# Performance work log

Hardware: AMD Instinct MI355X
Metric: run time of the kernel (lower is better)

Reference implementation:

```python
import jax, jax.numpy as jnp
import numpy as np

MARGIN = 0.5
N_CLASSES = 100

def setup_inputs() -> dict:
    key = jax.random.key(0)
    k1, k2 = jax.random.split(key)
    n, d = 8192, 128
    inputs = jax.random.normal(k1, (n, d), dtype=jnp.float32)
    targets = jax.random.randint(k2, (n,), 0, N_CLASSES, dtype=jnp.int64)
    return {"inputs": inputs, "targets": targets}

def reference(inputs, targets):
    # pairwise squared euclidean distances: [n, n]
    sq = jnp.sum(inputs * inputs, axis=1)  # [n]
    dist = sq[:, None] + sq[None, :] - 2.0 * (inputs @ inputs.T)
    dist = jnp.maximum(dist, 0.0)
    # positive mask: same label (diagonal included, matching original)
    mask = targets[:, None] == targets[None, :]  # [n, n] bool
    big = jnp.float32(1e30)
    dist_ap = jnp.max(jnp.where(mask, dist, -big), axis=1)  # hardest positive per row
    dist_an = jnp.min(jnp.where(mask, big, dist), axis=1)   # hardest negative per row
    loss = jnp.sum(jax.nn.relu(dist_ap - dist_an + MARGIN))
    return loss
```

## Files before the change

### kernel.cpp

```cpp
#include <hip/hip_runtime.h>
#include <hip/hip_bf16.h>

#define D 128
#define MARGIN 0.5f
#define NSPLIT 16
#define JSPAN 512

typedef __attribute__((ext_vector_type(8))) short bf16x8;
typedef __attribute__((ext_vector_type(4))) float f32x4;

__global__ void prep_kernel(const float* __restrict__ x,
                            float* __restrict__ sq,
                            unsigned* __restrict__ ap,
                            unsigned* __restrict__ an,
                            __hip_bfloat16* __restrict__ xb,
                            float* __restrict__ out, int n) {
    int tid = threadIdx.x;
    int row = blockIdx.x * 4 + (tid >> 6);
    int lane = tid & 63;
    const float2* xr = (const float2*)(x + (size_t)row * D);
    float2 v = xr[lane];
    __hip_bfloat162 b2;
    b2.x = __float2bfloat16(v.x);
    b2.y = __float2bfloat16(v.y);
    ((__hip_bfloat162*)(xb + (size_t)row * D))[lane] = b2;
    float s = v.x * v.x + v.y * v.y;
    #pragma unroll
    for (int o = 32; o > 0; o >>= 1) s += __shfl_xor(s, o, 64);
    if (lane == 0) {
        sq[row] = s;
        ap[row] = 0u;
        an[row] = 0x7F800000u;
    }
    if (blockIdx.x == 0 && tid == 0) *out = 0.0f;
}

__launch_bounds__(256, 4)
__global__ void gram_kernel(const __hip_bfloat16* __restrict__ xb,
                            const float* __restrict__ sq,
                            const int* __restrict__ tgt,
                            unsigned* __restrict__ ap,
                            unsigned* __restrict__ an, int n) {
    __shared__ __align__(16) __hip_bfloat16 Bs[2][64 * D];
    __shared__ float sqs[JSPAN];
    __shared__ int   tgs[JSPAN];

    const int tid  = threadIdx.x;
    const int wid  = tid >> 6;
    const int lane = tid & 63;
    const int quad = lane >> 4;
    const int l    = lane & 15;
    const int i0   = blockIdx.x * 128;
    const int jspan = n / NSPLIT;
    const int njit  = jspan / 64;
    const int j0    = blockIdx.y * jspan;
    const int rowbase = i0 + wid * 32;

    bf16x8 afrag[2][4];
    {
        const __hip_bfloat16* abase = xb + (size_t)(rowbase + l) * D + quad * 8;
        #pragma unroll
        for (int mt = 0; mt < 2; ++mt)
            #pragma unroll
            for (int ks = 0; ks < 4; ++ks)
                afrag[mt][ks] = *(const bf16x8*)(abase + (size_t)mt * 16 * D + ks * 32);
    }

    int li[2][4];
    #pragma unroll
    for (int mt = 0; mt < 2; ++mt)
        #pragma unroll
        for (int reg = 0; reg < 4; ++reg)
            li[mt][reg] = tgt[rowbase + mt * 16 + quad * 4 + reg];

    float lap[8], lan[8];
    #pragma unroll
    for (int k = 0; k < 8; ++k) { lap[k] = -1e30f; lan[k] = 1e30f; }

    const int q0 = wid * 256;
    const char* xbb = (const char*)xb;

    #define PREFETCH(jt0, buf)                                                \
        do {                                                                  \
            _Pragma("unroll")                                                 \
            for (int i_ = 0; i_ < 4; ++i_) {                                  \
                int q_ = q0 + i_ * 64 + lane;                                 \
                int r_ = q_ >> 4;                                             \
                int c_ = (q_ & 15) ^ (r_ & 15);                               \
                const char* g_ = xbb + (size_t)((jt0) + r_) * 256             \
                                     + (size_t)c_ * 16;                       \
                char* l_ = (char*)&Bs[buf][0] + (size_t)(q0 + i_ * 64) * 16;  \
                __builtin_amdgcn_global_load_lds(                             \
                    (const __attribute__((address_space(1))) void*)g_,        \
                    (__attribute__((address_space(3))) void*)l_, 16, 0, 0);   \
            }                                                                 \
        } while (0)

    PREFETCH(j0, 0);
    sqs[tid]       = sq[j0 + tid];
    sqs[tid + 256] = sq[j0 + tid + 256];
    tgs[tid]       = tgt[j0 + tid];
    tgs[tid + 256] = tgt[j0 + tid + 256];
    __syncthreads();

    for (int jj = 0; jj < njit; ++jj) {
        const int cur = jj & 1;
        if (jj < njit - 1) PREFETCH(j0 + (jj + 1) * 64, cur ^ 1);

        const char* Bb = (const char*)&Bs[cur][0];
        const int jb = jj * 64;
        #pragma unroll
        for (int jt = 0; jt < 4; ++jt) {
            f32x4 acc0 = (f32x4){0.f, 0.f, 0.f, 0.f};
            f32x4 acc1 = (f32x4){0.f, 0.f, 0.f, 0.f};
            #pragma unroll
            for (int ks = 0; ks < 4; ++ks) {
                int q = (jt * 16 + l) * 16 + ((ks * 4 + quad) ^ l);
                bf16x8 bfr = *(const bf16x8*)(Bb + (size_t)q * 16);
                acc0 = __builtin_amdgcn_mfma_f32_16x16x32_bf16(afrag[0][ks], bfr, acc0, 0, 0, 0);
                acc1 = __builtin_amdgcn_mfma_f32_16x16x32_bf16(afrag[1][ks], bfr, acc1, 0, 0, 0);
            }
            float sjc = sqs[jb + jt * 16 + l];
            int   tjc = tgs[jb + jt * 16 + l];
            #pragma unroll
            for (int reg = 0; reg < 4; ++reg) {
                float t0 = fmaf(-2.0f, acc0[reg], sjc);
                float t1 = fmaf(-2.0f, acc1[reg], sjc);
                bool s0 = (li[0][reg] == tjc);
                bool s1 = (li[1][reg] == tjc);
                lap[reg]     = fmaxf(lap[reg],     s0 ? t0 : -1e30f);
                lan[reg]     = fminf(lan[reg],     s0 ? 1e30f : t0);
                lap[4 + reg] = fmaxf(lap[4 + reg], s1 ? t1 : -1e30f);
                lan[4 + reg] = fminf(lan[4 + reg], s1 ? 1e30f : t1);
            }
        }

        __syncthreads();
    }
    #undef PREFETCH

    #pragma unroll
    for (int mt = 0; mt < 2; ++mt)
        #pragma unroll
        for (int reg = 0; reg < 4; ++reg) {
            float p = lap[mt * 4 + reg], q = lan[mt * 4 + reg];
            #pragma unroll
            for (int o = 1; o < 16; o <<= 1) {
                p = fmaxf(p, __shfl_xor(p, o, 64));
                q = fminf(q, __shfl_xor(q, o, 64));
            }
            if (l == mt * 4 + reg) {
                int gi = rowbase + mt * 16 + quad * 4 + reg;
                float s = sq[gi];
                atomicMax(&ap[gi], __float_as_uint(fmaxf(s + p, 0.0f)));
                atomicMin(&an[gi], __float_as_uint(fmaxf(s + q, 0.0f)));
            }
        }
}

__global__ void final_kernel(const unsigned* __restrict__ ap,
                             const unsigned* __restrict__ an,
                             float* __restrict__ out, int n) {
    int i = blockIdx.x * blockDim.x + threadIdx.x;
    float v = 0.f;
    if (i < n) {
        float p = __uint_as_float(ap[i]);
        float q = __uint_as_float(an[i]);
        v = fmaxf(p - q + MARGIN, 0.0f);
    }
    #pragma unroll
    for (int o = 32; o > 0; o >>= 1) v += __shfl_xor(v, o, 64);
    __shared__ float ws[4];
    int lane = threadIdx.x & 63, w = threadIdx.x >> 6;
    if (lane == 0) ws[w] = v;
    __syncthreads();
    if (threadIdx.x == 0) atomicAdd(out, ws[0] + ws[1] + ws[2] + ws[3]);
}

extern "C" void kernel_launch(void* const* d_in, const int* in_sizes, int n_in,
                              void* d_out, int out_size, void* d_ws, size_t ws_size,
                              hipStream_t stream) {
    const float* x   = (const float*)d_in[0];
    const int*   tgt = (const int*)d_in[1];
    float* out = (float*)d_out;
    const int n = in_sizes[1];

    float*          sq = (float*)d_ws;
    unsigned*       ap = (unsigned*)((char*)d_ws + (size_t)n * 4);
    unsigned*       an = ap + n;
    __hip_bfloat16* xb = (__hip_bfloat16*)((char*)d_ws + (size_t)n * 12);

    prep_kernel<<<n / 4, 256, 0, stream>>>(x, sq, ap, an, xb, out, n);
    dim3 grid(n / 128, NSPLIT);
    gram_kernel<<<grid, 256, 0, stream>>>(xb, sq, tgt, ap, an, n);
    final_kernel<<<n / 256, 256, 0, stream>>>(ap, an, out, n);
}
```

Measured before the change: 88.50 us.

## Use 4-stage 32-row LDS ring with fine-grained vmcnt waits and MFMA priority

Replaces the 2-buffer, 64-row double buffering with a 4-slot ring of 32-row tiles, prefetched three tiles ahead via global_load_lds. Explicit s_waitcnt vmcnt counts and raw s_barrier replace the per-iteration __syncthreads, so more loads stay in flight and barriers no longer drain all memory traffic. It also raises wave priority around the MFMA block with s_setprio. The loop count is hardcoded to 16 tiles of 32 rows, tying the kernel to n/NSPLIT == JSPAN == 512. The hand-written waitcnt counts must also match the compiler's actual instruction stream.

```diff
diff --git a/kernel.cpp b/kernel.cpp
--- a/kernel.cpp
+++ b/kernel.cpp
@@ -41,7 +41,7 @@
                             const int* __restrict__ tgt,
                             unsigned* __restrict__ ap,
                             unsigned* __restrict__ an, int n) {
-    __shared__ __align__(16) __hip_bfloat16 Bs[2][64 * D];
+    __shared__ __align__(16) __hip_bfloat16 Bs[4][32 * D];
     __shared__ float sqs[JSPAN];
     __shared__ int   tgs[JSPAN];
 
@@ -51,9 +51,7 @@
     const int quad = lane >> 4;
     const int l    = lane & 15;
     const int i0   = blockIdx.x * 128;
-    const int jspan = n / NSPLIT;
-    const int njit  = jspan / 64;
-    const int j0    = blockIdx.y * jspan;
+    const int j0   = blockIdx.y * JSPAN;
     const int rowbase = i0 + wid * 32;
 
     bf16x8 afrag[2][4];
@@ -77,67 +75,88 @@
     #pragma unroll
     for (int k = 0; k < 8; ++k) { lap[k] = -1e30f; lan[k] = 1e30f; }
 
-    const int q0 = wid * 256;
     const char* xbb = (const char*)xb;
 
-    #define PREFETCH(jt0, buf)                                                \
+    #define PREF_HALF(h)                                                      \
         do {                                                                  \
+            const int s_ = (h) & 3;                                           \
             _Pragma("unroll")                                                 \
-            for (int i_ = 0; i_ < 4; ++i_) {                                  \
-                int q_ = q0 + i_ * 64 + lane;                                 \
+            for (int i_ = 0; i_ < 2; ++i_) {                                  \
+                int q_ = wid * 128 + i_ * 64 + lane;                          \
                 int r_ = q_ >> 4;                                             \
                 int c_ = (q_ & 15) ^ (r_ & 15);                               \
-                const char* g_ = xbb + (size_t)((jt0) + r_) * 256             \
+                const char* g_ = xbb + (size_t)(j0 + (h) * 32 + r_) * 256     \
                                      + (size_t)c_ * 16;                       \
-                char* l_ = (char*)&Bs[buf][0] + (size_t)(q0 + i_ * 64) * 16;  \
+                char* l_ = (char*)Bs + (size_t)s_ * 8192                      \
+                         + (size_t)(wid * 128 + i_ * 64) * 16;                \
                 __builtin_amdgcn_global_load_lds(                             \
                     (const __attribute__((address_space(1))) void*)g_,        \
                     (__attribute__((address_space(3))) void*)l_, 16, 0, 0);   \
             }                                                                 \
         } while (0)
 
-    PREFETCH(j0, 0);
+    #define COMP_HALF(h)                                                      \
+        do {                                                                  \
+            const char* Bb_ = (const char*)Bs + (size_t)((h) & 3) * 8192;     \
+            _Pragma("unroll")                                                 \
+            for (int jt = 0; jt < 2; ++jt) {                                  \
+                f32x4 acc0 = (f32x4){0.f, 0.f, 0.f, 0.f};                     \
+                f32x4 acc1 = (f32x4){0.f, 0.f, 0.f, 0.f};                     \
+                __builtin_amdgcn_s_setprio(1);                                \
+                _Pragma("unroll")                                             \
+                for (int ks = 0; ks < 4; ++ks) {                              \
+                    int q = (jt * 16 + l) * 16 + ((ks * 4 + quad) ^ l);       \
+                    bf16x8 bfr = *(const bf16x8*)(Bb_ + (size_t)q * 16);      \
+                    acc0 = __builtin_amdgcn_mfma_f32_16x16x32_bf16(           \
+                        afrag[0][ks], bfr, acc0, 0, 0, 0);                    \
+                    acc1 = __builtin_amdgcn_mfma_f32_16x16x32_bf16(           \
+                        afrag[1][ks], bfr, acc1, 0, 0, 0);                    \
+                }                                                             \
+                __builtin_amdgcn_s_setprio(0);                                \
+                int jb_ = (h) * 32 + jt * 16;                                 \
+                float sjc = sqs[jb_ + l];                                     \
+                int   tjc = tgs[jb_ + l];                                     \
+                _Pragma("unroll")                                             \
+                for (int reg = 0; reg < 4; ++reg) {                           \
+                    float t0 = fmaf(-2.0f, acc0[reg], sjc);                   \
+                    float t1 = fmaf(-2.0f, acc1[reg], sjc);                   \
+                    bool s0 = (li[0][reg] == tjc);                            \
+                    bool s1 = (li[1][reg] == tjc);                            \
+                    lap[reg]     = fmaxf(lap[reg],     s0 ? t0 : -1e30f);     \
+                    lan[reg]     = fminf(lan[reg],     s0 ? 1e30f : t0);      \
+                    lap[4 + reg] = fmaxf(lap[4 + reg], s1 ? t1 : -1e30f);     \
+                    lan[4 + reg] = fminf(lan[4 + reg], s1 ? 1e30f : t1);      \
+                }                                                             \
+            }                                                                 \
+        } while (0)
+
+    PREF_HALF(0);
+    PREF_HALF(1);
+    PREF_HALF(2);
     sqs[tid]       = sq[j0 + tid];
     sqs[tid + 256] = sq[j0 + tid + 256];
     tgs[tid]       = tgt[j0 + tid];
     tgs[tid + 256] = tgt[j0 + tid + 256];
-    __syncthreads();
-
-    for (int jj = 0; jj < njit; ++jj) {
-        const int cur = jj & 1;
-        if (jj < njit - 1) PREFETCH(j0 + (jj + 1) * 64, cur ^ 1);
-
-        const char* Bb = (const char*)&Bs[cur][0];
-        const int jb = jj * 64;
-        #pragma unroll
-        for (int jt = 0; jt < 4; ++jt) {
-            f32x4 acc0 = (f32x4){0.f, 0.f, 0.f, 0.f};
-            f32x4 acc1 = (f32x4){0.f, 0.f, 0.f, 0.f};
-            #pragma unroll
-            for (int ks = 0; ks < 4; ++ks) {
-                int q = (jt * 16 + l) * 16 + ((ks * 4 + quad) ^ l);
-                bf16x8 bfr = *(const bf16x8*)(Bb + (size_t)q * 16);
-                acc0 = __builtin_amdgcn_mfma_f32_16x16x32_bf16(afrag[0][ks], bfr, acc0, 0, 0, 0);
-                acc1 = __builtin_amdgcn_mfma_f32_16x16x32_bf16(afrag[1][ks], bfr, acc1, 0, 0, 0);
-            }
-            float sjc = sqs[jb + jt * 16 + l];
-            int   tjc = tgs[jb + jt * 16 + l];
-            #pragma unroll
-            for (int reg = 0; reg < 4; ++reg) {
-                float t0 = fmaf(-2.0f, acc0[reg], sjc);
-                float t1 = fmaf(-2.0f, acc1[reg], sjc);
-                bool s0 = (li[0][reg] == tjc);
-                bool s1 = (li[1][reg] == tjc);
-                lap[reg]     = fmaxf(lap[reg],     s0 ? t0 : -1e30f);
-                lan[reg]     = fminf(lan[reg],     s0 ? 1e30f : t0);
-                lap[4 + reg] = fmaxf(lap[4 + reg], s1 ? t1 : -1e30f);
-                lan[4 + reg] = fminf(lan[4 + reg], s1 ? 1e30f : t1);
-            }
-        }
-
-        __syncthreads();
-    }
-    #undef PREFETCH
+    asm volatile("s_waitcnt lgkmcnt(0)" ::: "memory");
+
+    for (int h = 0; h < 14; ++h) {
+        asm volatile("s_waitcnt vmcnt(4)" ::: "memory");
+        __builtin_amdgcn_s_barrier();
+        asm volatile("" ::: "memory");
+        if (h < 13) PREF_HALF(h + 3);
+        COMP_HALF(h);
+    }
+    asm volatile("s_waitcnt vmcnt(2)" ::: "memory");
+    __builtin_amdgcn_s_barrier();
+    asm volatile("" ::: "memory");
+    COMP_HALF(14);
+    asm volatile("s_waitcnt vmcnt(0)" ::: "memory");
+    __builtin_amdgcn_s_barrier();
+    asm volatile("" ::: "memory");
+    COMP_HALF(15);
+
+    #undef PREF_HALF
+    #undef COMP_HALF
 
     #pragma unroll
     for (int mt = 0; mt < 2; ++mt)
```

New measurement: 86.67 us. 2.1% less time.

## Load B fragments directly from global memory and replace atomics with per-split partials

Applied to the files above, without the earlier changes.

Drops the LDS double-buffered B tile and its per-iteration barrier. Each wave now reads its B fragments straight from global memory (expected to hit L2, since the bf16 matrix is small), processing 32 columns per iteration with interleaved MFMAs under raised wave priority. The global atomicMax/atomicMin on ap/an are replaced by plain stores into per-split partial arrays, which the final kernel reduces across the 16 splits. The cost is redundant global/L2 traffic, because the four waves in a block each reload the same B rows, plus a larger workspace.

```diff
diff --git a/kernel.cpp b/kernel.cpp
--- a/kernel.cpp
+++ b/kernel.cpp
@@ -11,8 +11,6 @@
 
 __global__ void prep_kernel(const float* __restrict__ x,
                             float* __restrict__ sq,
-                            unsigned* __restrict__ ap,
-                            unsigned* __restrict__ an,
                             __hip_bfloat16* __restrict__ xb,
                             float* __restrict__ out, int n) {
     int tid = threadIdx.x;
@@ -27,11 +25,7 @@
     float s = v.x * v.x + v.y * v.y;
     #pragma unroll
     for (int o = 32; o > 0; o >>= 1) s += __shfl_xor(s, o, 64);
-    if (lane == 0) {
-        sq[row] = s;
-        ap[row] = 0u;
-        an[row] = 0x7F800000u;
-    }
+    if (lane == 0) sq[row] = s;
     if (blockIdx.x == 0 && tid == 0) *out = 0.0f;
 }
 
@@ -39,9 +33,8 @@
 __global__ void gram_kernel(const __hip_bfloat16* __restrict__ xb,
                             const float* __restrict__ sq,
                             const int* __restrict__ tgt,
-                            unsigned* __restrict__ ap,
-                            unsigned* __restrict__ an, int n) {
-    __shared__ __align__(16) __hip_bfloat16 Bs[2][64 * D];
+                            float* __restrict__ pap,
+                            float* __restrict__ pan, int n) {
     __shared__ float sqs[JSPAN];
     __shared__ int   tgs[JSPAN];
 
@@ -51,10 +44,13 @@
     const int quad = lane >> 4;
     const int l    = lane & 15;
     const int i0   = blockIdx.x * 128;
-    const int jspan = n / NSPLIT;
-    const int njit  = jspan / 64;
-    const int j0    = blockIdx.y * jspan;
+    const int j0   = blockIdx.y * JSPAN;
     const int rowbase = i0 + wid * 32;
+
+    sqs[tid]       = sq[j0 + tid];
+    sqs[tid + 256] = sq[j0 + tid + 256];
+    tgs[tid]       = tgt[j0 + tid];
+    tgs[tid + 256] = tgt[j0 + tid + 256];
 
     bf16x8 afrag[2][4];
     {
@@ -77,67 +73,53 @@
     #pragma unroll
     for (int k = 0; k < 8; ++k) { lap[k] = -1e30f; lan[k] = 1e30f; }
 
-    const int q0 = wid * 256;
-    const char* xbb = (const char*)xb;
-
-    #define PREFETCH(jt0, buf)                                                \
-        do {                                                                  \
-            _Pragma("unroll")                                                 \
-            for (int i_ = 0; i_ < 4; ++i_) {                                  \
-                int q_ = q0 + i_ * 64 + lane;                                 \
-                int r_ = q_ >> 4;                                             \
-                int c_ = (q_ & 15) ^ (r_ & 15);                               \
-                const char* g_ = xbb + (size_t)((jt0) + r_) * 256             \
-                                     + (size_t)c_ * 16;                       \
-                char* l_ = (char*)&Bs[buf][0] + (size_t)(q0 + i_ * 64) * 16;  \
-                __builtin_amdgcn_global_load_lds(                             \
-                    (const __attribute__((address_space(1))) void*)g_,        \
-                    (__attribute__((address_space(3))) void*)l_, 16, 0, 0);   \
-            }                                                                 \
-        } while (0)
-
-    PREFETCH(j0, 0);
-    sqs[tid]       = sq[j0 + tid];
-    sqs[tid + 256] = sq[j0 + tid + 256];
-    tgs[tid]       = tgt[j0 + tid];
-    tgs[tid + 256] = tgt[j0 + tid + 256];
     __syncthreads();
 
-    for (int jj = 0; jj < njit; ++jj) {
-        const int cur = jj & 1;
-        if (jj < njit - 1) PREFETCH(j0 + (jj + 1) * 64, cur ^ 1);
+    const char* xbb = (const char*)xb + (size_t)j0 * 256;
 
-        const char* Bb = (const char*)&Bs[cur][0];
-        const int jb = jj * 64;
+    for (int it = 0; it < 16; ++it) {
+        const int jb = it * 32;
+        bf16x8 bfr[2][4];
         #pragma unroll
-        for (int jt = 0; jt < 4; ++jt) {
-            f32x4 acc0 = (f32x4){0.f, 0.f, 0.f, 0.f};
-            f32x4 acc1 = (f32x4){0.f, 0.f, 0.f, 0.f};
+        for (int sub = 0; sub < 2; ++sub)
             #pragma unroll
-            for (int ks = 0; ks < 4; ++ks) {
-                int q = (jt * 16 + l) * 16 + ((ks * 4 + quad) ^ l);
-                bf16x8 bfr = *(const bf16x8*)(Bb + (size_t)q * 16);
-                acc0 = __builtin_amdgcn_mfma_f32_16x16x32_bf16(afrag[0][ks], bfr, acc0, 0, 0, 0);
-                acc1 = __builtin_amdgcn_mfma_f32_16x16x32_bf16(afrag[1][ks], bfr, acc1, 0, 0, 0);
-            }
-            float sjc = sqs[jb + jt * 16 + l];
-            int   tjc = tgs[jb + jt * 16 + l];
+            for (int ks = 0; ks < 4; ++ks)
+                bfr[sub][ks] = *(const bf16x8*)(
+                    xbb + (size_t)(jb + sub * 16 + l) * 256 + (ks * 4 + quad) * 16);
+
+        f32x4 acc[2][2];
+        #pragma unroll
+        for (int sub = 0; sub < 2; ++sub)
             #pragma unroll
-            for (int reg = 0; reg < 4; ++reg) {
-                float t0 = fmaf(-2.0f, acc0[reg], sjc);
-                float t1 = fmaf(-2.0f, acc1[reg], sjc);
-                bool s0 = (li[0][reg] == tjc);
-                bool s1 = (li[1][reg] == tjc);
-                lap[reg]     = fmaxf(lap[reg],     s0 ? t0 : -1e30f);
-                lan[reg]     = fminf(lan[reg],     s0 ? 1e30f : t0);
-                lap[4 + reg] = fmaxf(lap[4 + reg], s1 ? t1 : -1e30f);
-                lan[4 + reg] = fminf(lan[4 + reg], s1 ? 1e30f : t1);
-            }
+            for (int mt = 0; mt < 2; ++mt)
+                acc[sub][mt] = (f32x4){0.f, 0.f, 0.f, 0.f};
+
+        __builtin_amdgcn_s_setprio(1);
+        #pragma unroll
+        for (int ks = 0; ks < 4; ++ks)
+            #pragma unroll
+            for (int sub = 0; sub < 2; ++sub)
+                #pragma unroll
+                for (int mt = 0; mt < 2; ++mt)
+                    acc[sub][mt] = __builtin_amdgcn_mfma_f32_16x16x32_bf16(
+                        afrag[mt][ks], bfr[sub][ks], acc[sub][mt], 0, 0, 0);
+        __builtin_amdgcn_s_setprio(0);
+
+        #pragma unroll
+        for (int sub = 0; sub < 2; ++sub) {
+            float sjc = sqs[jb + sub * 16 + l];
+            int   tjc = tgs[jb + sub * 16 + l];
+            #pragma unroll
+            for (int mt = 0; mt < 2; ++mt)
+                #pragma unroll
+                for (int reg = 0; reg < 4; ++reg) {
+                    float t0 = fmaf(-2.0f, acc[sub][mt][reg], sjc);
+                    bool s0 = (li[mt][reg] == tjc);
+                    lap[mt * 4 + reg] = fmaxf(lap[mt * 4 + reg], s0 ? t0 : -1e30f);
+                    lan[mt * 4 + reg] = fminf(lan[mt * 4 + reg], s0 ? 1e30f : t0);
+                }
         }
-
-        __syncthreads();
     }
-    #undef PREFETCH
 
     #pragma unroll
     for (int mt = 0; mt < 2; ++mt)
@@ -152,22 +134,23 @@
             if (l == mt * 4 + reg) {
                 int gi = rowbase + mt * 16 + quad * 4 + reg;
                 float s = sq[gi];
-                atomicMax(&ap[gi], __float_as_uint(fmaxf(s + p, 0.0f)));
-                atomicMin(&an[gi], __float_as_uint(fmaxf(s + q, 0.0f)));
+                pap[(size_t)blockIdx.y * n + gi] = fmaxf(s + p, 0.0f);
+                pan[(size_t)blockIdx.y * n + gi] = fmaxf(s + q, 0.0f);
             }
         }
 }
 
-__global__ void final_kernel(const unsigned* __restrict__ ap,
-                             const unsigned* __restrict__ an,
+__global__ void final_kernel(const float* __restrict__ pap,
+                             const float* __restrict__ pan,
                              float* __restrict__ out, int n) {
     int i = blockIdx.x * blockDim.x + threadIdx.x;
-    float v = 0.f;
-    if (i < n) {
-        float p = __uint_as_float(ap[i]);
-        float q = __uint_as_float(an[i]);
-        v = fmaxf(p - q + MARGIN, 0.0f);
+    float p = pap[i], q = pan[i];
+    #pragma unroll
+    for (int s = 1; s < NSPLIT; ++s) {
+        p = fmaxf(p, pap[(size_t)s * n + i]);
+        q = fminf(q, pan[(size_t)s * n + i]);
     }
+    float v = fmaxf(p - q + MARGIN, 0.0f);
     #pragma unroll
     for (int o = 32; o > 0; o >>= 1) v += __shfl_xor(v, o, 64);
     __shared__ float ws[4];
@@ -185,13 +168,13 @@
     float* out = (float*)d_out;
     const int n = in_sizes[1];
 
-    float*          sq = (float*)d_ws;
-    unsigned*       ap = (unsigned*)((char*)d_ws + (size_t)n * 4);
-    unsigned*       an = ap + n;
-    __hip_bfloat16* xb = (__hip_bfloat16*)((char*)d_ws + (size_t)n * 12);
+    float*          sq  = (float*)d_ws;
+    float*          pap = (float*)((char*)d_ws + (size_t)n * 4);
+    float*          pan = (float*)((char*)d_ws + (size_t)n * 4 + (size_t)n * NSPLIT * 4);
+    __hip_bfloat16* xb  = (__hip_bfloat16*)((char*)d_ws + (size_t)n * 4 + (size_t)n * NSPLIT * 8);
 
-    prep_kernel<<<n / 4, 256, 0, stream>>>(x, sq, ap, an, xb, out, n);
+    prep_kernel<<<n / 4, 256, 0, stream>>>(x, sq, xb, out, n);
     dim3 grid(n / 128, NSPLIT);
-    gram_kernel<<<grid, 256, 0, stream>>>(xb, sq, tgt, ap, an, n);
-    final_kernel<<<n / 256, 256, 0, stream>>>(ap, an, out, n);
+    gram_kernel<<<grid, 256, 0, stream>>>(xb, sq, tgt, pap, pan, n);
+    final_kernel<<<n / 256, 256, 0, stream>>>(pap, pan, out, n);
 }
```

Result: slower. 124.2 us (+40.3%).
